# Kernel optimization log

Hardware: AMD Instinct MI355X
Metric: run time of the kernel (lower is better)

## Reference

```python
import jax, jax.numpy as jnp
import numpy as np

SEMA_DIM = 1024
L1, L2, B = 256, 320, 64


def setup_inputs() -> dict:
    key = jax.random.key(0)
    k1, k2, kw1, kb1, kw2, kb2 = jax.random.split(key, 6)
    D = SEMA_DIM
    s = 1.0 / np.sqrt(D)
    return {
        "r1": jax.random.normal(k1, (L1, B, D), dtype=jnp.float32),
        "r2": jax.random.normal(k2, (L2, B, D), dtype=jnp.float32),
        "W1": jax.random.uniform(kw1, (D, D), jnp.float32, -s, s),
        "b1": jax.random.uniform(kb1, (D,), jnp.float32, -s, s),
        "W2": jax.random.uniform(kw2, (D, D), jnp.float32, -s, s),
        "b2": jax.random.uniform(kb2, (D,), jnp.float32, -s, s),
    }


def _mlp(x, W1, b1, W2, b2):
    # torch Linear: x @ W.T + b
    h = jax.nn.relu(x @ W1.T + b1)
    return h @ W2.T + b2


def reference(r1, r2, W1, b1, W2, b2):
    # (L, B, D) -> mlp -> (B, L, D)
    r1 = jnp.transpose(_mlp(r1, W1, b1, W2, b2), (1, 0, 2))  # [B, L1, D]
    r2 = jnp.transpose(_mlp(r2, W1, b1, W2, b2), (1, 0, 2))  # [B, L2, D]

    o = jnp.einsum("bid,bjd->bij", r1, r2)  # [B, L1, L2]
    o1 = jax.nn.softmax(o, axis=2)           # attend r1 -> r2
    o2 = jax.nn.softmax(o, axis=1)           # attend r2 -> r1

    r1_c = jnp.einsum("bij,bjd->bid", o1, r2)  # [B, L1, D]
    r2_c = jnp.einsum("bij,bid->bjd", o2, r1)  # [B, L2, D]

    r1_pool = jnp.concatenate([r1, r1_c], axis=-1).sum(axis=1) / r1.shape[1]  # [B, 2D]
    r2_pool = jnp.concatenate([r2, r2_c], axis=-1).sum(axis=1) / r2.shape[1]  # [B, 2D]
    return (r1_pool, r2_pool)
```

## Files before the change

kernel.cpp:

```cpp
#include <hip/hip_runtime.h>
#include <stdint.h>

#define L1C 256
#define L2C 320
#define BC  64
#define DC  1024

typedef __bf16 bf16_t;
typedef __bf16 bf16x8 __attribute__((ext_vector_type(8)));
typedef __bf16 bf16x4 __attribute__((ext_vector_type(4)));
typedef float  f32x4  __attribute__((ext_vector_type(4)));

__device__ __forceinline__ void gload16(const void* g, void* l) {
  __builtin_amdgcn_global_load_lds(
      (__attribute__((address_space(1))) void*)g,
      (__attribute__((address_space(3))) void*)l, 16, 0, 0);
}

__global__ __launch_bounds__(256)
void conv_kernel(const float* __restrict__ src, bf16_t* __restrict__ dst, int n4) {
  int i = blockIdx.x * 256 + threadIdx.x;
  const int stride = gridDim.x * 256;
  for (; i < n4; i += stride) {
    float4 v = ((const float4*)src)[i];
    bf16x4 o = { (__bf16)v.x, (__bf16)v.y, (__bf16)v.z, (__bf16)v.w };
    ((bf16x4*)dst)[i] = o;
  }
}

__global__ __launch_bounds__(256)
void w2t_kernel(const float* __restrict__ W2, bf16_t* __restrict__ W2T) {
  __shared__ float tile[32][33];
  const int tx = threadIdx.x & 31, ty = threadIdx.x >> 5;
  const int x0 = blockIdx.x * 32, y0 = blockIdx.y * 32;
#pragma unroll
  for (int k = 0; k < 32; k += 8)
    tile[ty + k][tx] = W2[(size_t)(y0 + ty + k) * 1024 + x0 + tx];
  __syncthreads();
#pragma unroll
  for (int k = 0; k < 32; k += 8)
    W2T[(size_t)(x0 + ty + k) * 1024 + y0 + tx] = (bf16_t)tile[tx][ty + k];
}

__global__ __launch_bounds__(256)
void wb_kernel(const float* __restrict__ W2, const float* __restrict__ b2,
               float* __restrict__ w2b) {
  const int dt = threadIdx.x & 15, kg = threadIdx.x >> 4;
  const int d = blockIdx.x * 16 + dt;
  float s = 0.f;
  for (int k = kg * 64; k < kg * 64 + 64; ++k)
    s += W2[(size_t)k * 1024 + d] * b2[k];
  __shared__ float red[16][17];
  red[kg][dt] = s;
  __syncthreads();
  if (kg == 0) {
    float t = 0.f;
#pragma unroll
    for (int g = 0; g < 16; ++g) t += red[g][dt];
    w2b[d] = t;
  }
}

__global__ __launch_bounds__(512, 2)
void mlp_gemm8(const bf16_t* __restrict__ A, const bf16_t* __restrict__ W,
               const float* __restrict__ bias, bf16_t* __restrict__ C,
               int Mtiles, int relu, const float* __restrict__ w2b,
               float* __restrict__ tT1, float* __restrict__ tT2) {
  const int nwg = Mtiles * 4;
  const int cpx = nwg >> 3;
  const int wg  = ((int)blockIdx.x & 7) * cpx + ((int)blockIdx.x >> 3);
  const int mt = wg >> 2, nt = wg & 3;

  __shared__ __align__(16) char lds[131072];

  const int t    = threadIdx.x;
  const int lane = t & 63, wid = t >> 6;
  const int wm = wid >> 2, wn = wid & 3;
  const int rsel = lane & 15, hi = lane >> 4;
  const int t16 = t * 16;

  const int P0 = t16, P1 = 8192 + t16;
  const int Lg0 = P0 ^ ((P0 >> 3) & 0x30);
  const int Lg1 = P1 ^ ((P1 >> 3) & 0x30);
  const int rS0 = Lg0 >> 6, cS0 = (Lg0 & 63) >> 1;
  const int rS1 = Lg1 >> 6, cS1 = (Lg1 & 63) >> 1;
  const bf16_t* pA0 = A + (size_t)(mt * 256 + rS0) * 1024 + cS0;
  const bf16_t* pA1 = A + (size_t)(mt * 256 + rS1) * 1024 + cS1;
  const bf16_t* pB0 = W + (size_t)(nt * 256 + rS0) * 1024 + cS0;
  const bf16_t* pB1 = W + (size_t)(nt * 256 + rS1) * 1024 + cS1;

  const int kchunk = (hi ^ ((rsel >> 1) & 3)) << 4;
  const int offA = ((wm * 128 + rsel) << 6) + kchunk;
  const int offB = 16384 + ((wn * 64 + rsel) << 6) + kchunk;

  f32x4 acc[8][4] = {};
  bf16x8 bfr[4];

#pragma unroll
  for (int p = 0; p < 3; ++p) {
    char* db = lds + p * 32768;
    gload16(pA0 + p * 32, db + t16);
    gload16(pA1 + p * 32, db + 8192 + t16);
    gload16(pB0 + p * 32, db + 16384 + t16);
    gload16(pB1 + p * 32, db + 24576 + t16);
  }
  asm volatile("s_waitcnt vmcnt(8)" ::: "memory");
  __builtin_amdgcn_s_barrier();
  __builtin_amdgcn_sched_barrier(0);

#pragma unroll 1
  for (int tt = 0; tt < 32; ++tt) {
    const char* rb = lds + (tt & 3) * 32768;
    char* sb = lds + ((tt + 3) & 3) * 32768;
    const int ks = (tt + 3) * 32;
    bf16x8 af[4];
#pragma unroll
    for (int m = 0; m < 4; ++m) af[m] = *(const bf16x8*)(rb + offA + m * 1024);
#pragma unroll
    for (int n = 0; n < 4; ++n) bfr[n] = *(const bf16x8*)(rb + offB + n * 1024);
    if (tt < 29) {
      gload16(pA0 + ks, sb + t16);
      gload16(pA1 + ks, sb + 8192 + t16);
    }
    __builtin_amdgcn_s_setprio(1);
#pragma unroll
    for (int m = 0; m < 4; ++m)
#pragma unroll
      for (int n = 0; n < 4; ++n)
        acc[m][n] = __builtin_amdgcn_mfma_f32_16x16x32_bf16(af[m], bfr[n], acc[m][n], 0, 0, 0);
    __builtin_amdgcn_s_setprio(0);
    __builtin_amdgcn_s_barrier();
    __builtin_amdgcn_sched_barrier(0);
#pragma unroll
    for (int m = 0; m < 4; ++m) af[m] = *(const bf16x8*)(rb + offA + (m + 4) * 1024);
    if (tt < 29) {
      gload16(pB0 + ks, sb + 16384 + t16);
      gload16(pB1 + ks, sb + 24576 + t16);
    }
    __builtin_amdgcn_s_setprio(1);
#pragma unroll
    for (int m = 0; m < 4; ++m)
#pragma unroll
      for (int n = 0; n < 4; ++n)
        acc[m + 4][n] = __builtin_amdgcn_mfma_f32_16x16x32_bf16(af[m], bfr[n], acc[m + 4][n], 0, 0, 0);
    __builtin_amdgcn_s_setprio(0);
    if (tt < 29)       asm volatile("s_waitcnt vmcnt(8)" ::: "memory");
    else if (tt == 29) asm volatile("s_waitcnt vmcnt(4)" ::: "memory");
    else if (tt == 30) asm volatile("s_waitcnt vmcnt(0)" ::: "memory");
    __builtin_amdgcn_s_barrier();
    __builtin_amdgcn_sched_barrier(0);
  }

  const int row0 = mt * 256 + wm * 128 + hi * 4;
  const int col0 = nt * 256 + wn * 64 + rsel;
  float bv[4];
#pragma unroll
  for (int n = 0; n < 4; ++n) bv[n] = bias[col0 + n * 16];
#pragma unroll
  for (int m = 0; m < 8; ++m) {
#pragma unroll
    for (int q = 0; q < 4; ++q) {
      const size_t rr = (size_t)(row0 + m * 16 + q) * 1024;
#pragma unroll
      for (int n = 0; n < 4; ++n) {
        float v = acc[m][n][q] + bv[n];
        if (relu) v = fmaxf(v, 0.f);
        C[rr + col0 + n * 16] = (bf16_t)v;
      }
    }
  }

  if (w2b) {
    float wv[4];
#pragma unroll
    for (int n = 0; n < 4; ++n) wv[n] = w2b[col0 + n * 16];
#pragma unroll
    for (int m = 0; m < 8; ++m) {
#pragma unroll
      for (int q = 0; q < 4; ++q) {
        float s = 0.f;
#pragma unroll
        for (int n = 0; n < 4; ++n) {
          float v = acc[m][n][q] + bv[n];
          if (relu) v = fmaxf(v, 0.f);
          v = (float)(bf16_t)v;
          s += v * wv[n];
        }
        s += __shfl_xor(s, 1);
        s += __shfl_xor(s, 2);
        s += __shfl_xor(s, 4);
        s += __shfl_xor(s, 8);
        if (rsel == 0) {
          const int r = row0 + m * 16 + q;
          if (r < 16384) atomicAdd(&tT1[(r & 63) * L1C + (r >> 6)], s);
          else {
            const int r2 = r - 16384;
            atomicAdd(&tT2[(r2 & 63) * L2C + (r2 >> 6)], s);
          }
        }
      }
    }
  }
}

__global__ __launch_bounds__(256)
void gemmK(const bf16_t* __restrict__ A, const bf16_t* __restrict__ W,
           float* __restrict__ P, int KS) {
  const int slice = (int)blockIdx.x >> 6;
  const int tl = (int)blockIdx.x & 63;
  const int mt = tl >> 3, nt = tl & 7;
  const int koff = slice * KS;

  const int f = threadIdx.x;
  const int lane = f & 63, w = f >> 6;
  const int sRow = f >> 2, sCol8 = (f & 3) * 8;

  const bf16_t* Ab = A + (size_t)mt * 128 * 1024 + (size_t)sRow * 1024 + sCol8;
  const bf16_t* Bb = W + (size_t)nt * 128 * 1024 + (size_t)sRow * 1024 + sCol8;

  __shared__ __align__(16) bf16_t sA[128 * 32];
  __shared__ __align__(16) bf16_t sB[128 * 32];
  bf16_t* sAp = sA + sRow * 32 + sCol8;
  bf16_t* sBp = sB + sRow * 32 + sCol8;

  const int wr = (w >> 1) * 64, wc = (w & 1) * 64;
  const int rsel = lane & 15, koff2 = (lane >> 4) * 8;
  const bf16_t* rA = sA + (wr + rsel) * 32 + koff2;
  const bf16_t* rB = sB + (wc + rsel) * 32 + koff2;

  f32x4 acc[4][4] = {};
  for (int kt = koff; kt < koff + KS; kt += 32) {
    __syncthreads();
    gload16(Ab + kt,             sAp);
    gload16(Ab + kt + 64 * 1024, sAp + 64 * 32);
    gload16(Bb + kt,             sBp);
    gload16(Bb + kt + 64 * 1024, sBp + 64 * 32);
    asm volatile("s_waitcnt vmcnt(0)" ::: "memory");
    __syncthreads();
    bf16x8 af[4], bfv[4];
#pragma unroll
    for (int m = 0; m < 4; ++m) af[m] = *(const bf16x8*)(rA + m * 16 * 32);
#pragma unroll
    for (int n = 0; n < 4; ++n) bfv[n] = *(const bf16x8*)(rB + n * 16 * 32);
#pragma unroll
    for (int m = 0; m < 4; ++m)
#pragma unroll
      for (int n = 0; n < 4; ++n)
        acc[m][n] = __builtin_amdgcn_mfma_f32_16x16x32_bf16(af[m], bfv[n], acc[m][n], 0, 0, 0);
  }

  float* Pb = P + (size_t)slice * 1048576;
  const int row0 = mt * 128 + wr + (lane >> 4) * 4;
  const int col0 = nt * 128 + wc + rsel;
#pragma unroll
  for (int n = 0; n < 4; ++n) {
    const int c = col0 + n * 16;
#pragma unroll
    for (int m = 0; m < 4; ++m) {
      const int r = row0 + m * 16;
#pragma unroll
      for (int q = 0; q < 4; ++q)
        Pb[(size_t)(r + q) * 1024 + c] = acc[m][n][q];
    }
  }
}

__global__ __launch_bounds__(256)
void g_reduce(const float* __restrict__ Gp, bf16_t* __restrict__ GB) {
  const int i4 = blockIdx.x * 256 + threadIdx.x;
  float4 a = ((const float4*)Gp)[i4];
  float4 b = ((const float4*)(Gp + 1048576))[i4];
  float4 c = ((const float4*)(Gp + 2097152))[i4];
  float4 d = ((const float4*)(Gp + 3145728))[i4];
  bf16x4 o = { (bf16_t)(a.x + b.x + c.x + d.x), (bf16_t)(a.y + b.y + c.y + d.y),
               (bf16_t)(a.z + b.z + c.z + d.z), (bf16_t)(a.w + b.w + c.w + d.w) };
  ((bf16x4*)GB)[i4] = o;
}

__global__ __launch_bounds__(256)
void pool_gemmK(const bf16_t* __restrict__ A, const bf16_t* __restrict__ W,
                float* __restrict__ P) {
  const int slice = (int)blockIdx.x >> 4;
  const int tl = (int)blockIdx.x & 15;
  const int mt = tl >> 3, nt = tl & 7;
  const int koff = slice * 128;

  const int f = threadIdx.x;
  const int lane = f & 63, w = f >> 6;
  const int sRow = f >> 2, sCol8 = (f & 3) * 8;

  const bf16_t* Ab = A + (size_t)mt * 128 * 1024 + (size_t)sRow * 1024 + sCol8;
  const bf16_t* Bb = W + (size_t)nt * 128 * 1024 + (size_t)sRow * 1024 + sCol8;

  __shared__ __align__(16) bf16_t sA[128 * 32];
  __shared__ __align__(16) bf16_t sB[128 * 32];
  bf16_t* sAp = sA + sRow * 32 + sCol8;
  bf16_t* sBp = sB + sRow * 32 + sCol8;

  const int wr = (w >> 1) * 64, wc = (w & 1) * 64;
  const int rsel = lane & 15, koff2 = (lane >> 4) * 8;
  const bf16_t* rA = sA + (wr + rsel) * 32 + koff2;
  const bf16_t* rB = sB + (wc + rsel) * 32 + koff2;

  f32x4 acc[4][4] = {};
  for (int kt = koff; kt < koff + 128; kt += 32) {
    __syncthreads();
    gload16(Ab + kt,             sAp);
    gload16(Ab + kt + 64 * 1024, sAp + 64 * 32);
    gload16(Bb + kt,             sBp);
    gload16(Bb + kt + 64 * 1024, sBp + 64 * 32);
    asm volatile("s_waitcnt vmcnt(0)" ::: "memory");
    __syncthreads();
    bf16x8 af[4], bfv[4];
#pragma unroll
    for (int m = 0; m < 4; ++m) af[m] = *(const bf16x8*)(rA + m * 16 * 32);
#pragma unroll
    for (int n = 0; n < 4; ++n) bfv[n] = *(const bf16x8*)(rB + n * 16 * 32);
#pragma unroll
    for (int m = 0; m < 4; ++m)
#pragma unroll
      for (int n = 0; n < 4; ++n)
        acc[m][n] = __builtin_amdgcn_mfma_f32_16x16x32_bf16(af[m], bfv[n], acc[m][n], 0, 0, 0);
  }

  float* Pb = P + (size_t)slice * 262144;
  const int row0 = mt * 128 + wr + (lane >> 4) * 4;
  const int col0 = nt * 128 + wc + rsel;
#pragma unroll
  for (int n = 0; n < 4; ++n) {
    const int c = col0 + n * 16;
#pragma unroll
    for (int m = 0; m < 4; ++m) {
      const int r = row0 + m * 16;
#pragma unroll
      for (int q = 0; q < 4; ++q)
        Pb[(size_t)(r + q) * 1024 + c] = acc[m][n][q];
    }
  }
}

__global__ __launch_bounds__(256)
void pool_reduce(const float* __restrict__ Pp, const float* __restrict__ b2,
                 float* __restrict__ out) {
  const int idx = blockIdx.x * 256 + threadIdx.x;
  const int r = idx >> 10, c = idx & 1023;
  float s = b2[c];
#pragma unroll
  for (int sl = 0; sl < 8; ++sl) s += Pp[(size_t)sl * 262144 + idx];
  const int g = r >> 6, b = r & 63;
  out[(size_t)(g >> 1) * 131072 + (size_t)b * 2048 + (g & 1) * 1024 + c] = s;
}

__global__ __launch_bounds__(256)
void logits_gemm(const bf16_t* __restrict__ Y1, const bf16_t* __restrict__ Y2,
                 float* __restrict__ O) {
  const int wg = ((int)blockIdx.x & 7) * 48 + ((int)blockIdx.x >> 3);
  const int b = wg / 6, t = wg % 6;
  const int mt = t / 3, nt = t % 3;

  const int f = threadIdx.x;
  const int lane = f & 63, w = f >> 6;
  const int sRow = f >> 2, sCol8 = (f & 3) * 8;

  const int i0 = mt * 128 + sRow;
  const int i1 = i0 + 64;
  int j0 = nt * 128 + sRow;      if (j0 > L2C - 1) j0 = L2C - 1;
  int j1 = nt * 128 + sRow + 64; if (j1 > L2C - 1) j1 = L2C - 1;
  const bf16_t* A0 = Y1 + ((size_t)i0 * BC + b) * DC + sCol8;
  const bf16_t* A1 = Y1 + ((size_t)i1 * BC + b) * DC + sCol8;
  const bf16_t* B0 = Y2 + ((size_t)j0 * BC + b) * DC + sCol8;
  const bf16_t* B1 = Y2 + ((size_t)j1 * BC + b) * DC + sCol8;

  __shared__ __align__(16) bf16_t sA[128 * 32];
  __shared__ __align__(16) bf16_t sB[128 * 32];
  bf16_t* sAp = sA + sRow * 32 + sCol8;
  bf16_t* sBp = sB + sRow * 32 + sCol8;

  const int wr = (w >> 1) * 64, wc = (w & 1) * 64;
  const int rsel = lane & 15, koff = (lane >> 4) * 8;
  const bf16_t* rA = sA + (wr + rsel) * 32 + koff;
  const bf16_t* rB = sB + (wc + rsel) * 32 + koff;

  f32x4 acc[4][4] = {};
  for (int kt = 0; kt < 1024; kt += 32) {
    __syncthreads();
    gload16(A0 + kt, sAp);
    gload16(A1 + kt, sAp + 64 * 32);
    gload16(B0 + kt, sBp);
    gload16(B1 + kt, sBp + 64 * 32);
    asm volatile("s_waitcnt vmcnt(0)" ::: "memory");
    __syncthreads();
    bf16x8 af[4], bfv[4];
#pragma unroll
    for (int m = 0; m < 4; ++m) af[m] = *(const bf16x8*)(rA + m * 16 * 32);
#pragma unroll
    for (int n = 0; n < 4; ++n) bfv[n] = *(const bf16x8*)(rB + n * 16 * 32);
#pragma unroll
    for (int m = 0; m < 4; ++m)
#pragma unroll
      for (int n = 0; n < 4; ++n)
        acc[m][n] = __builtin_amdgcn_mfma_f32_16x16x32_bf16(af[m], bfv[n], acc[m][n], 0, 0, 0);
  }

  float* Ob = O + (size_t)b * L1C * L2C;
  const int row0 = mt * 128 + wr + (lane >> 4) * 4;
  const int col0 = nt * 128 + wc + rsel;
#pragma unroll
  for (int n = 0; n < 4; ++n) {
    const int c = col0 + n * 16;
    if (c < L2C) {
#pragma unroll
      for (int m = 0; m < 4; ++m) {
        const int r = row0 + m * 16;
#pragma unroll
        for (int q = 0; q < 4; ++q)
          Ob[(size_t)(r + q) * L2C + c] = acc[m][n][q];
      }
    }
  }
}

__global__ __launch_bounds__(256)
void row_stats(const float* __restrict__ O, const float* __restrict__ tT2,
               float* __restrict__ rowM, float* __restrict__ rowInv) {
  const int gw = blockIdx.x * 4 + (threadIdx.x >> 6);
  const int lane = threadIdx.x & 63;
  const int b = gw >> 8;
  const float* row = O + (size_t)gw * L2C;
  const float* t2 = tT2 + b * L2C;
  float v[5];
  float m = -1e30f;
#pragma unroll
  for (int t = 0; t < 5; ++t) { v[t] = row[t * 64 + lane] + t2[t * 64 + lane]; m = fmaxf(m, v[t]); }
#pragma unroll
  for (int off = 32; off; off >>= 1) m = fmaxf(m, __shfl_xor(m, off));
  float s = 0.f;
#pragma unroll
  for (int t = 0; t < 5; ++t) s += __expf(v[t] - m);
#pragma unroll
  for (int off = 32; off; off >>= 1) s += __shfl_xor(s, off);
  if (lane == 0) { rowM[gw] = m; rowInv[gw] = 1.f / s; }
}

__global__ __launch_bounds__(256)
void col_stats_c1(const float* __restrict__ O, const float* __restrict__ tT1,
                  const float* __restrict__ tT2,
                  const float* __restrict__ rowM, const float* __restrict__ rowInv,
                  float* __restrict__ colM, float* __restrict__ colInv,
                  float* __restrict__ c1) {
  const int b = blockIdx.x / 5, jb = blockIdx.x % 5;
  const int jl = threadIdx.x & 63, ig = threadIdx.x >> 6;
  const int j = jb * 64 + jl;
  const float* Ob = O + (size_t)b * L1C * L2C + j;
  const float* rM = rowM + b * L1C;
  const float* rI = rowInv + b * L1C;
  const float* t1 = tT1 + b * L1C;
  const float t2j = tT2[b * L2C + j];
  float m = -1e30f, s = 0.f, cp = 0.f;
  for (int i = ig; i < L1C; i += 4) {
    float ov = Ob[(size_t)i * L2C];
    float v = ov + t1[i];
    float mn = fmaxf(m, v);
    s = s * __expf(m - mn) + __expf(v - mn);
    m = mn;
    cp += __expf(ov + t2j - rM[i]) * rI[i];
  }
  __shared__ float sm[4][64], ss[4][64], sc[4][64];
  sm[ig][jl] = m; ss[ig][jl] = s; sc[ig][jl] = cp;
  __syncthreads();
  if (ig == 0) {
    for (int g = 1; g < 4; ++g) {
      float mg = sm[g][jl], sg = ss[g][jl];
      float mn = fmaxf(m, mg);
      s = s * __expf(m - mn) + sg * __expf(mg - mn);
      m = mn;
      cp += sc[g][jl];
    }
    colM[b * L2C + j] = m;
    colInv[b * L2C + j] = 1.f / s;
    c1[b * L2C + j] = cp;
  }
}

__global__ __launch_bounds__(256)
void c2_kernel(const float* __restrict__ O, const float* __restrict__ tT1,
               const float* __restrict__ colM, const float* __restrict__ colInv,
               float* __restrict__ c2) {
  const int gw = blockIdx.x * 4 + (threadIdx.x >> 6);
  const int lane = threadIdx.x & 63;
  const int b = gw >> 8;
  const float* row = O + (size_t)gw * L2C;
  const float* cM = colM + b * L2C;
  const float* cI = colInv + b * L2C;
  const float t1i = tT1[b * L1C + (gw & 255)];
  float s = 0.f;
#pragma unroll
  for (int t = 0; t < 5; ++t) {
    const int j = t * 64 + lane;
    s += __expf(row[j] + t1i - cM[j]) * cI[j];
  }
#pragma unroll
  for (int off = 32; off; off >>= 1) s += __shfl_xor(s, off);
  if (lane == 0) c2[gw] = s;
}

__global__ __launch_bounds__(256)
void u_kernel(const bf16_t* __restrict__ H, const float* __restrict__ c1,
              const float* __restrict__ c2, bf16_t* __restrict__ Ub) {
  const int b = blockIdx.x >> 2;
  const int d = (blockIdx.x & 3) * 256 + threadIdx.x;
  const bf16_t* H2 = H + (size_t)L1C * BC * DC;
  float s1 = 0.f, s1c = 0.f, s2 = 0.f, s2c = 0.f;
  const float* c2b = c2 + b * L1C;
  for (int i = 0; i < L1C; ++i) {
    float v = (float)H[((size_t)i * BC + b) * DC + d];
    s1 += v; s1c += c2b[i] * v;
  }
  const float* c1b = c1 + b * L2C;
  for (int j = 0; j < L2C; ++j) {
    float v = (float)H2[((size_t)j * BC + b) * DC + d];
    s2 += v; s2c += c1b[j] * v;
  }
  Ub[(size_t)(0 * 64 + b) * 1024 + d] = (bf16_t)(s1  * (1.f / L1C));
  Ub[(size_t)(1 * 64 + b) * 1024 + d] = (bf16_t)(s2c * (1.f / L1C));
  Ub[(size_t)(2 * 64 + b) * 1024 + d] = (bf16_t)(s2  * (1.f / L2C));
  Ub[(size_t)(3 * 64 + b) * 1024 + d] = (bf16_t)(s1c * (1.f / L2C));
}

extern "C" void kernel_launch(void* const* d_in, const int* in_sizes, int n_in,
                              void* d_out, int out_size, void* d_ws, size_t ws_size,
                              hipStream_t stream) {
  const float* r1 = (const float*)d_in[0];
  const float* r2 = (const float*)d_in[1];
  const float* W1 = (const float*)d_in[2];
  const float* b1 = (const float*)d_in[3];
  const float* W2 = (const float*)d_in[4];
  const float* b2 = (const float*)d_in[5];
  float* out = (float*)d_out;
  char* ws = (char*)d_ws;

  const size_t M1 = (size_t)L1C * BC;
  const size_t M2 = (size_t)L2C * BC;
  const size_t Mt = M1 + M2;

  size_t off = 0;
  bf16_t* XB  = (bf16_t*)(ws + off); off += Mt * DC * 2;
  bf16_t* HB  = (bf16_t*)(ws + off); off += Mt * DC * 2;
  bf16_t* WB1 = (bf16_t*)(ws + off); off += (size_t)DC * DC * 2;
  bf16_t* WB2 = (bf16_t*)(ws + off); off += (size_t)DC * DC * 2;
  bf16_t* W2T = (bf16_t*)(ws + off); off += (size_t)DC * DC * 2;
  bf16_t* GB  = (bf16_t*)(ws + off); off += (size_t)DC * DC * 2;
  float* w2b   = (float*)(ws + off); off += 4096;
  float* zb    = (float*)(ws + off); off += 4096;
  float* tT1   = (float*)(ws + off); off += BC * L1C * 4;
  float* tT2   = (float*)(ws + off); off += BC * L2C * 4;
  float* rowM  = (float*)(ws + off); off += BC * L1C * 4;
  float* rowIv = (float*)(ws + off); off += BC * L1C * 4;
  float* colM  = (float*)(ws + off); off += BC * L2C * 4;
  float* colIv = (float*)(ws + off); off += BC * L2C * 4;
  float* c1v   = (float*)(ws + off); off += BC * L2C * 4;
  float* c2v   = (float*)(ws + off); off += BC * L1C * 4;
  bf16_t* Ub   = (bf16_t*)(ws + off); off += 256 * DC * 2;

  bf16_t* Z = XB;
  float*  O = (float*)((char*)XB + 35651584);
  float*  Gpart = (float*)((char*)XB + 58720256);
  float*  Ppart = (float*)HB;
  bf16_t* H2 = HB + M1 * DC;

  conv_kernel<<<2048, 256, 0, stream>>>(r1, XB,           (int)(M1 * DC / 4));
  conv_kernel<<<2048, 256, 0, stream>>>(r2, XB + M1 * DC, (int)(M2 * DC / 4));
  conv_kernel<<<512,  256, 0, stream>>>(W1, WB1, (int)((size_t)DC * DC / 4));
  conv_kernel<<<512,  256, 0, stream>>>(W2, WB2, (int)((size_t)DC * DC / 4));
  w2t_kernel<<<dim3(32, 32), 256, 0, stream>>>(W2, W2T);
  wb_kernel<<<64, 256, 0, stream>>>(W2, b2, w2b);
  hipMemsetAsync(zb, 0, 4096, stream);
  hipMemsetAsync(tT1, 0, BC * L1C * 4, stream);
  hipMemsetAsync(tT2, 0, BC * L2C * 4, stream);

  mlp_gemm8<<<576, 512, 0, stream>>>(XB, WB1, b1, HB, 144, 1, w2b, tT1, tT2);

  gemmK<<<256, 256, 0, stream>>>(W2T, W2T, Gpart, 256);
  g_reduce<<<1024, 256, 0, stream>>>(Gpart, GB);

  mlp_gemm8<<<256, 512, 0, stream>>>(HB, GB, zb, Z, 64, 0, nullptr, nullptr, nullptr);

  logits_gemm<<<384, 256, 0, stream>>>(Z, H2, O);

  row_stats<<<4096, 256, 0, stream>>>(O, tT2, rowM, rowIv);
  col_stats_c1<<<320, 256, 0, stream>>>(O, tT1, tT2, rowM, rowIv, colM, colIv, c1v);
  c2_kernel<<<4096, 256, 0, stream>>>(O, tT1, colM, colIv, c2v);

  u_kernel<<<256, 256, 0, stream>>>(HB, c1v, c2v, Ub);
  pool_gemmK<<<128, 256, 0, stream>>>(Ub, WB2, Ppart);
  pool_reduce<<<1024, 256, 0, stream>>>(Ppart, b2, out);
}
```

Before: 336.4 us.

## Fuse fp32-to-bf16 activation conversion into first MLP GEMM, move row-dot to separate kernel

Result: faster. 307.0 us (-8.7%).

```diff
diff --git a/kernel.cpp b/kernel.cpp
--- a/kernel.cpp
+++ b/kernel.cpp
@@ -62,10 +62,136 @@
 }
 
 __global__ __launch_bounds__(512, 2)
+void mlp_gemm_f32a(const float* __restrict__ R1, const float* __restrict__ R2,
+                   const bf16_t* __restrict__ W, const float* __restrict__ bias,
+                   bf16_t* __restrict__ C, int Mtiles) {
+  const int nwg = Mtiles * 4;
+  const int cpx = nwg >> 3;
+  const int wg  = ((int)blockIdx.x & 7) * cpx + ((int)blockIdx.x >> 3);
+  const int mt = wg >> 2, nt = wg & 3;
+
+  __shared__ __align__(16) char lds[147456];
+
+  const int t    = threadIdx.x;
+  const int lane = t & 63, wid = t >> 6;
+  const int wm = wid >> 2, wn = wid & 3;
+  const int rsel = lane & 15, hi = lane >> 4;
+  const int t16 = t * 16;
+
+  const int rT = t >> 3;
+  const int gT = (t & 7) ^ (rT & 7);
+  const float* Abase = (mt < 64) ? (R1 + (size_t)mt * 256 * 1024)
+                                 : (R2 + (size_t)(mt - 64) * 256 * 1024);
+  const float* pA[4];
+#pragma unroll
+  for (int l = 0; l < 4; ++l)
+    pA[l] = Abase + (size_t)(l * 64 + rT) * 1024 + gT * 4;
+
+  const int P0 = t16, P1 = 8192 + t16;
+  const int Lg0 = P0 ^ ((P0 >> 3) & 0x30);
+  const int Lg1 = P1 ^ ((P1 >> 3) & 0x30);
+  const bf16_t* pB0 = W + (size_t)(nt * 256 + (Lg0 >> 6)) * 1024 + ((Lg0 & 63) >> 1);
+  const bf16_t* pB1 = W + (size_t)(nt * 256 + (Lg1 >> 6)) * 1024 + ((Lg1 & 63) >> 1);
+
+  const int rowA = wm * 128 + rsel;
+  const int offA0 = (rowA << 7) + (((2 * hi)     ^ (rsel & 7)) << 4);
+  const int offA1 = (rowA << 7) + (((2 * hi + 1) ^ (rsel & 7)) << 4);
+  const int kchunk = (hi ^ ((rsel >> 1) & 3)) << 4;
+  const int offB = 32768 + ((wn * 64 + rsel) << 6) + kchunk;
+
+  f32x4 acc[8][4] = {};
+  bf16x8 bfr[4];
+
+#pragma unroll
+  for (int p = 0; p < 2; ++p) {
+    char* db = lds + p * 49152;
+#pragma unroll
+    for (int l = 0; l < 4; ++l) gload16(pA[l] + p * 32, db + l * 8192 + t16);
+    gload16(pB0 + p * 32, db + 32768 + t16);
+    gload16(pB1 + p * 32, db + 40960 + t16);
+  }
+  asm volatile("s_waitcnt vmcnt(6)" ::: "memory");
+  __builtin_amdgcn_s_barrier();
+  __builtin_amdgcn_sched_barrier(0);
+
+  int cur = 0;
+#pragma unroll 1
+  for (int tt = 0; tt < 32; ++tt) {
+    const char* rb = lds + cur * 49152;
+    int nx = cur + 2; if (nx >= 3) nx -= 3;
+    char* sb = lds + nx * 49152;
+    const int ks = (tt + 2) * 32;
+    bf16x8 af[4];
+#pragma unroll
+    for (int m = 0; m < 4; ++m) {
+      f32x4 a0 = *(const f32x4*)(rb + offA0 + m * 2048);
+      f32x4 a1 = *(const f32x4*)(rb + offA1 + m * 2048);
+      af[m] = bf16x8{ (bf16_t)a0[0], (bf16_t)a0[1], (bf16_t)a0[2], (bf16_t)a0[3],
+                      (bf16_t)a1[0], (bf16_t)a1[1], (bf16_t)a1[2], (bf16_t)a1[3] };
+    }
+#pragma unroll
+    for (int n = 0; n < 4; ++n) bfr[n] = *(const bf16x8*)(rb + offB + n * 1024);
+    if (tt < 30) {
+#pragma unroll
+      for (int l = 0; l < 4; ++l) gload16(pA[l] + ks, sb + l * 8192 + t16);
+    }
+    __builtin_amdgcn_s_setprio(1);
+#pragma unroll
+    for (int m = 0; m < 4; ++m)
+#pragma unroll
+      for (int n = 0; n < 4; ++n)
+        acc[m][n] = __builtin_amdgcn_mfma_f32_16x16x32_bf16(af[m], bfr[n], acc[m][n], 0, 0, 0);
+    __builtin_amdgcn_s_setprio(0);
+    __builtin_amdgcn_s_barrier();
+    __builtin_amdgcn_sched_barrier(0);
+#pragma unroll
+    for (int m = 0; m < 4; ++m) {
+      f32x4 a0 = *(const f32x4*)(rb + offA0 + (m + 4) * 2048);
+      f32x4 a1 = *(const f32x4*)(rb + offA1 + (m + 4) * 2048);
+      af[m] = bf16x8{ (bf16_t)a0[0], (bf16_t)a0[1], (bf16_t)a0[2], (bf16_t)a0[3],
+                      (bf16_t)a1[0], (bf16_t)a1[1], (bf16_t)a1[2], (bf16_t)a1[3] };
+    }
+    if (tt < 30) {
+      gload16(pB0 + ks, sb + 32768 + t16);
+      gload16(pB1 + ks, sb + 40960 + t16);
+    }
+    __builtin_amdgcn_s_setprio(1);
+#pragma unroll
+    for (int m = 0; m < 4; ++m)
+#pragma unroll
+      for (int n = 0; n < 4; ++n)
+        acc[m + 4][n] = __builtin_amdgcn_mfma_f32_16x16x32_bf16(af[m], bfr[n], acc[m + 4][n], 0, 0, 0);
+    __builtin_amdgcn_s_setprio(0);
+    if (tt < 30)       asm volatile("s_waitcnt vmcnt(6)" ::: "memory");
+    else if (tt == 30) asm volatile("s_waitcnt vmcnt(0)" ::: "memory");
+    __builtin_amdgcn_s_barrier();
+    __builtin_amdgcn_sched_barrier(0);
+    cur = (cur + 1 == 3) ? 0 : cur + 1;
+  }
+
+  const int row0 = mt * 256 + wm * 128 + hi * 4;
+  const int col0 = nt * 256 + wn * 64 + rsel;
+  float bv[4];
+#pragma unroll
+  for (int n = 0; n < 4; ++n) bv[n] = bias[col0 + n * 16];
+#pragma unroll
+  for (int m = 0; m < 8; ++m) {
+#pragma unroll
+    for (int q = 0; q < 4; ++q) {
+      const size_t rr = (size_t)(row0 + m * 16 + q) * 1024;
+#pragma unroll
+      for (int n = 0; n < 4; ++n) {
+        float v = fmaxf(acc[m][n][q] + bv[n], 0.f);
+        C[rr + col0 + n * 16] = (bf16_t)v;
+      }
+    }
+  }
+}
+
+__global__ __launch_bounds__(512, 2)
 void mlp_gemm8(const bf16_t* __restrict__ A, const bf16_t* __restrict__ W,
                const float* __restrict__ bias, bf16_t* __restrict__ C,
-               int Mtiles, int relu, const float* __restrict__ w2b,
-               float* __restrict__ tT1, float* __restrict__ tT2) {
+               int Mtiles, int relu) {
   const int nwg = Mtiles * 4;
   const int cpx = nwg >> 3;
   const int wg  = ((int)blockIdx.x & 7) * cpx + ((int)blockIdx.x >> 3);
@@ -166,38 +292,6 @@
         float v = acc[m][n][q] + bv[n];
         if (relu) v = fmaxf(v, 0.f);
         C[rr + col0 + n * 16] = (bf16_t)v;
-      }
-    }
-  }
-
-  if (w2b) {
-    float wv[4];
-#pragma unroll
-    for (int n = 0; n < 4; ++n) wv[n] = w2b[col0 + n * 16];
-#pragma unroll
-    for (int m = 0; m < 8; ++m) {
-#pragma unroll
-      for (int q = 0; q < 4; ++q) {
-        float s = 0.f;
-#pragma unroll
-        for (int n = 0; n < 4; ++n) {
-          float v = acc[m][n][q] + bv[n];
-          if (relu) v = fmaxf(v, 0.f);
-          v = (float)(bf16_t)v;
-          s += v * wv[n];
-        }
-        s += __shfl_xor(s, 1);
-        s += __shfl_xor(s, 2);
-        s += __shfl_xor(s, 4);
-        s += __shfl_xor(s, 8);
-        if (rsel == 0) {
-          const int r = row0 + m * 16 + q;
-          if (r < 16384) atomicAdd(&tT1[(r & 63) * L1C + (r >> 6)], s);
-          else {
-            const int r2 = r - 16384;
-            atomicAdd(&tT2[(r2 & 63) * L2C + (r2 >> 6)], s);
-          }
-        }
       }
     }
   }
@@ -349,6 +443,28 @@
   for (int sl = 0; sl < 8; ++sl) s += Pp[(size_t)sl * 262144 + idx];
   const int g = r >> 6, b = r & 63;
   out[(size_t)(g >> 1) * 131072 + (size_t)b * 2048 + (g & 1) * 1024 + c] = s;
+}
+
+__global__ __launch_bounds__(256)
+void t_kernel(const bf16_t* __restrict__ H, const float* __restrict__ w2b,
+              float* __restrict__ tT1, float* __restrict__ tT2) {
+  const int wv = threadIdx.x >> 6, lane = threadIdx.x & 63;
+  const int r = blockIdx.x * 4 + wv;
+  const bf16_t* hrow = H + (size_t)r * 1024;
+  float s = 0.f;
+#pragma unroll
+  for (int h = 0; h < 2; ++h) {
+    bf16x8 v = *(const bf16x8*)(hrow + h * 512 + lane * 8);
+#pragma unroll
+    for (int e = 0; e < 8; ++e) s += (float)v[e] * w2b[h * 512 + lane * 8 + e];
+  }
+#pragma unroll
+  for (int off = 32; off; off >>= 1) s += __shfl_xor(s, off);
+  if (lane == 0) {
+    const int b = r & 63;
+    if (r < 16384) tT1[b * L1C + (r >> 6)] = s;
+    else           tT2[b * L2C + ((r - 16384) >> 6)] = s;
+  }
 }
 
 __global__ __launch_bounds__(256)
@@ -568,22 +684,19 @@
   float*  Ppart = (float*)HB;
   bf16_t* H2 = HB + M1 * DC;
 
-  conv_kernel<<<2048, 256, 0, stream>>>(r1, XB,           (int)(M1 * DC / 4));
-  conv_kernel<<<2048, 256, 0, stream>>>(r2, XB + M1 * DC, (int)(M2 * DC / 4));
-  conv_kernel<<<512,  256, 0, stream>>>(W1, WB1, (int)((size_t)DC * DC / 4));
-  conv_kernel<<<512,  256, 0, stream>>>(W2, WB2, (int)((size_t)DC * DC / 4));
+  conv_kernel<<<512, 256, 0, stream>>>(W1, WB1, (int)((size_t)DC * DC / 4));
+  conv_kernel<<<512, 256, 0, stream>>>(W2, WB2, (int)((size_t)DC * DC / 4));
   w2t_kernel<<<dim3(32, 32), 256, 0, stream>>>(W2, W2T);
   wb_kernel<<<64, 256, 0, stream>>>(W2, b2, w2b);
-  hipMemsetAsync(zb, 0, 4096, stream);
-  hipMemsetAsync(tT1, 0, BC * L1C * 4, stream);
-  hipMemsetAsync(tT2, 0, BC * L2C * 4, stream);
-
-  mlp_gemm8<<<576, 512, 0, stream>>>(XB, WB1, b1, HB, 144, 1, w2b, tT1, tT2);
+  (void)hipMemsetAsync(zb, 0, 4096, stream);
+
+  mlp_gemm_f32a<<<576, 512, 0, stream>>>(r1, r2, WB1, b1, HB, 144);
 
   gemmK<<<256, 256, 0, stream>>>(W2T, W2T, Gpart, 256);
+  t_kernel<<<9216, 256, 0, stream>>>(HB, w2b, tT1, tT2);
   g_reduce<<<1024, 256, 0, stream>>>(Gpart, GB);
 
-  mlp_gemm8<<<256, 512, 0, stream>>>(HB, GB, zb, Z, 64, 0, nullptr, nullptr, nullptr);
+  mlp_gemm8<<<256, 512, 0, stream>>>(HB, GB, zb, Z, 64, 0);
 
   logits_gemm<<<384, 256, 0, stream>>>(Z, H2, O);
 
```
